# Performance work log

Hardware: AMD Instinct MI355X
Metric: run time of the kernel (lower is better)

Reference implementation:

```python
import jax, jax.numpy as jnp
import numpy as np

# LSNNParameters defaults (norse)
TAU_SYN_INV = 200.0     # 1/tau_syn
TAU_MEM_INV = 100.0     # 1/tau_mem
TAU_ADAPT_INV = 1.0 / 800.0  # 1/tau_adapt
V_LEAK = 0.0
V_TH = 1.0
V_RESET = 0.0
BETA = 1.8
DT = 0.001

B, IN_F, OUT_F = 8192, 512, 1024


def setup_inputs() -> dict:
    key = jax.random.key(0)
    k0, k1, k2, k3, k4, k5, k6 = jax.random.split(key, 7)
    input_spikes = (jax.random.uniform(k0, (B, IN_F)) < 0.2).astype(jnp.float32)
    z = (jax.random.uniform(k1, (B, OUT_F)) < 0.2).astype(jnp.float32)
    v = jax.random.normal(k2, (B, OUT_F)) * 0.5
    i = jax.random.normal(k3, (B, OUT_F)) * 0.5
    b = jax.random.uniform(k4, (B, OUT_F))
    input_weights = jax.random.normal(k5, (OUT_F, IN_F)) / np.sqrt(IN_F)
    recurrent_weights = jax.random.normal(k6, (OUT_F, OUT_F))
    return {
        "input_spikes": input_spikes,
        "z": z,
        "v": v,
        "i": i,
        "b": b,
        "input_weights": input_weights,
        "recurrent_weights": recurrent_weights,
    }


def reference(input_spikes, z, v, i, b, input_weights, recurrent_weights):
    # One euler step of the LSNN cell (norse lsnn_step).
    # voltage update: dv = dt * tau_mem_inv * ((v_leak - v) + i)
    v_decayed = v + DT * TAU_MEM_INV * ((V_LEAK - v) + i)
    # current decay: di = -dt * tau_syn_inv * i
    i_decayed = i + DT * (-TAU_SYN_INV) * i
    # adaptive threshold relaxes toward v_th
    b_decayed = b + DT * TAU_ADAPT_INV * (V_TH - b)
    # spike condition (heaviside jump)
    z_new = (v_decayed - b_decayed > 0).astype(v.dtype)
    # reset
    v_new = (1.0 - z_new) * v_decayed + z_new * V_RESET
    # current jumps from input + recurrent synapses (x @ W^T, torch linear)
    i_new = (
        i_decayed
        + jnp.einsum("bi,oi->bo", input_spikes, input_weights)
        + jnp.einsum("bo,no->bn", z, recurrent_weights)
    )
    # threshold adaptation
    b_new = b_decayed + z_new * TAU_ADAPT_INV * BETA
    # stack (z, v, i, b) new state -> [4, B, OUT_F]
    return jnp.stack([z_new, v_new, i_new, b_new])
```

## Files before the change

kernel.cpp:

```cpp
#include <hip/hip_runtime.h>

#define B_ROWS 8192
#define IN_F 512
#define OUT_F 1024
#define K_TOT 1536

#define BM 64
#define BN 64
#define BK 64
#define NITER (K_TOT / BK)

#define A4_COUNT (B_ROWS * (K_TOT / 4))
#define W4_COUNT (OUT_F  * (K_TOT / 4))

typedef short bfrag __attribute__((ext_vector_type(8)));
typedef float f4    __attribute__((ext_vector_type(4)));

__device__ __forceinline__ unsigned int pack2bf(float a, float b) {
    unsigned int ua = __float_as_uint(a);
    unsigned int ub = __float_as_uint(b);
    ua = (ua + 0x7fffu + ((ua >> 16) & 1u)) >> 16;
    ub = (ub + 0x7fffu + ((ub >> 16) & 1u)) & 0xffff0000u;
    return ua | ub;
}

__global__ __launch_bounds__(256) void precast(
    const float* __restrict__ spikes, const float* __restrict__ zin,
    const float* __restrict__ Wi,     const float* __restrict__ Wr,
    unsigned short* __restrict__ Abf, unsigned short* __restrict__ Wbf)
{
    const int idx = blockIdx.x * 256 + threadIdx.x;
    const float* src;
    unsigned short* dst;
    if (idx < A4_COUNT) {
        const int row = idx / 384, c4 = idx - row * 384;
        src = (c4 < 128) ? spikes + (size_t)row * IN_F + c4 * 4
                         : zin    + (size_t)row * OUT_F + (c4 - 128) * 4;
        dst = Abf + (size_t)idx * 4;
    } else {
        const int w = idx - A4_COUNT;
        const int row = w / 384, c4 = w - row * 384;
        src = (c4 < 128) ? Wi + (size_t)row * IN_F + c4 * 4
                         : Wr + (size_t)row * OUT_F + (c4 - 128) * 4;
        dst = Wbf + (size_t)w * 4;
    }
    const float4 v = *(const float4*)src;
    uint2 pk = { pack2bf(v.x, v.y), pack2bf(v.z, v.w) };
    *(uint2*)dst = pk;
}

__global__ __launch_bounds__(256, 8) void lsnn_gemm(
    const unsigned short* __restrict__ Abf,
    const unsigned short* __restrict__ Wbf,
    const float* __restrict__ vin,
    const float* __restrict__ iin,
    const float* __restrict__ bin,
    float* __restrict__ out)
{
    __shared__ unsigned short As[BM * BK];
    __shared__ unsigned short Ws[BN * BK];

    const int tid = threadIdx.x;
    const int bid = blockIdx.x;
    const int n0 = (bid & 15) * BN;
    const int m0 = (bid >> 4) * BM;

    const int lane = tid & 63;
    const int wave = tid >> 6;
    const int wm = (wave >> 1) * 32;
    const int wn = (wave & 1) * 32;
    const int lr = lane & 15;
    const int lq = lane >> 4;

    f4 acc[2][2];
    #pragma unroll
    for (int a = 0; a < 2; ++a)
        #pragma unroll
        for (int b = 0; b < 2; ++b)
            acc[a][b] = (f4)0.0f;

    const unsigned short* Ab = Abf + (size_t)m0 * K_TOT;
    const unsigned short* Wb = Wbf + (size_t)n0 * K_TOT;

    for (int it = 0; it < NITER; ++it) {
        const int kt = it * BK;
        __syncthreads();

        #pragma unroll
        for (int p = 0; p < 2; ++p) {
            const int j0 = p * 256 + wave * 64;
            const int q  = j0 + lane;
            const int r = q >> 3, s = q & 7, c = s ^ (r & 7);
            __builtin_amdgcn_global_load_lds(
                (const __attribute__((address_space(1))) void*)(Ab + (size_t)r * K_TOT + kt + c * 8),
                (__attribute__((address_space(3))) void*)(As + j0 * 8),
                16, 0, 0);
        }
        #pragma unroll
        for (int p = 0; p < 2; ++p) {
            const int j0 = p * 256 + wave * 64;
            const int q  = j0 + lane;
            const int r = q >> 3, s = q & 7, c = s ^ (r & 7);
            __builtin_amdgcn_global_load_lds(
                (const __attribute__((address_space(1))) void*)(Wb + (size_t)r * K_TOT + kt + c * 8),
                (__attribute__((address_space(3))) void*)(Ws + j0 * 8),
                16, 0, 0);
        }
        __syncthreads();

        #pragma unroll
        for (int ks = 0; ks < 2; ++ks) {
            const int cc = ks * 4 + lq;
            bfrag af[2], wf[2];
            #pragma unroll
            for (int t = 0; t < 2; ++t) {
                const int row = wm + t * 16 + lr;
                af[t] = *(const bfrag*)&As[row * BK + (cc ^ (row & 7)) * 8];
            }
            #pragma unroll
            for (int t = 0; t < 2; ++t) {
                const int row = wn + t * 16 + lr;
                wf[t] = *(const bfrag*)&Ws[row * BK + (cc ^ (row & 7)) * 8];
            }
            #pragma unroll
            for (int tm = 0; tm < 2; ++tm)
                #pragma unroll
                for (int tn = 0; tn < 2; ++tn)
                    acc[tm][tn] = __builtin_amdgcn_mfma_f32_16x16x32_bf16(
                        af[tm], wf[tn], acc[tm][tn], 0, 0, 0);
        }
    }

    const size_t PL = (size_t)B_ROWS * OUT_F;
    #pragma unroll
    for (int tm = 0; tm < 2; ++tm) {
        #pragma unroll
        for (int tn = 0; tn < 2; ++tn) {
            #pragma unroll
            for (int r = 0; r < 4; ++r) {
                const int gm = m0 + wm + tm * 16 + lq * 4 + r;
                const int gn = n0 + wn + tn * 16 + lr;
                const size_t idx = (size_t)gm * OUT_F + gn;
                const float v = vin[idx];
                const float i = iin[idx];
                const float b = bin[idx];
                const float v_dec = v + 0.1f * ((0.0f - v) + i);
                const float i_dec = i - 0.2f * i;
                const float b_dec = b + 1.25e-06f * (1.0f - b);
                const float zn = (v_dec - b_dec > 0.0f) ? 1.0f : 0.0f;
                const float vn = (1.0f - zn) * v_dec;
                const float inew = i_dec + acc[tm][tn][r];
                const float bnew = b_dec + zn * 0.00225f;
                out[idx]          = zn;
                out[PL + idx]     = vn;
                out[2 * PL + idx] = inew;
                out[3 * PL + idx] = bnew;
            }
        }
    }
}

extern "C" void kernel_launch(void* const* d_in, const int* in_sizes, int n_in,
                              void* d_out, int out_size, void* d_ws, size_t ws_size,
                              hipStream_t stream) {
    const float* spikes = (const float*)d_in[0];
    const float* z      = (const float*)d_in[1];
    const float* v      = (const float*)d_in[2];
    const float* i      = (const float*)d_in[3];
    const float* b      = (const float*)d_in[4];
    const float* Wi     = (const float*)d_in[5];
    const float* Wr     = (const float*)d_in[6];
    float* out = (float*)d_out;

    unsigned short* Abf = (unsigned short*)d_ws;
    unsigned short* Wbf = Abf + (size_t)B_ROWS * K_TOT;

    const int pc_grid = (A4_COUNT + W4_COUNT) / 256;
    precast<<<pc_grid, 256, 0, stream>>>(spikes, z, Wi, Wr, Abf, Wbf);

    const int grid = (B_ROWS / BM) * (OUT_F / BN);
    lsnn_gemm<<<grid, 256, 0, stream>>>(Abf, Wbf, v, i, b, out);
}
```

Measured before the change: 312.8 us.

## Fuse activation bf16 cast into GEMM with register-prefetched double-buffered LDS

```diff
diff --git a/kernel.cpp b/kernel.cpp
--- a/kernel.cpp
+++ b/kernel.cpp
@@ -10,13 +10,12 @@
 #define BK 64
 #define NITER (K_TOT / BK)
 
-#define A4_COUNT (B_ROWS * (K_TOT / 4))
-#define W4_COUNT (OUT_F  * (K_TOT / 4))
+#define W4_COUNT (OUT_F * (K_TOT / 4))
 
 typedef short bfrag __attribute__((ext_vector_type(8)));
 typedef float f4    __attribute__((ext_vector_type(4)));
 
-__device__ __forceinline__ unsigned int pack2bf(float a, float b) {
+__device__ __forceinline__ unsigned int pack2bf_rne(float a, float b) {
     unsigned int ua = __float_as_uint(a);
     unsigned int ub = __float_as_uint(b);
     ua = (ua + 0x7fffu + ((ua >> 16) & 1u)) >> 16;
@@ -24,41 +23,34 @@
     return ua | ub;
 }
 
-__global__ __launch_bounds__(256) void precast(
-    const float* __restrict__ spikes, const float* __restrict__ zin,
-    const float* __restrict__ Wi,     const float* __restrict__ Wr,
-    unsigned short* __restrict__ Abf, unsigned short* __restrict__ Wbf)
+__device__ __forceinline__ unsigned int pack2bf_trunc(float a, float b) {
+    return (__float_as_uint(a) >> 16) | (__float_as_uint(b) & 0xffff0000u);
+}
+
+__global__ __launch_bounds__(256) void precast_w(
+    const float* __restrict__ Wi, const float* __restrict__ Wr,
+    unsigned short* __restrict__ Wbf)
 {
     const int idx = blockIdx.x * 256 + threadIdx.x;
-    const float* src;
-    unsigned short* dst;
-    if (idx < A4_COUNT) {
-        const int row = idx / 384, c4 = idx - row * 384;
-        src = (c4 < 128) ? spikes + (size_t)row * IN_F + c4 * 4
-                         : zin    + (size_t)row * OUT_F + (c4 - 128) * 4;
-        dst = Abf + (size_t)idx * 4;
-    } else {
-        const int w = idx - A4_COUNT;
-        const int row = w / 384, c4 = w - row * 384;
-        src = (c4 < 128) ? Wi + (size_t)row * IN_F + c4 * 4
-                         : Wr + (size_t)row * OUT_F + (c4 - 128) * 4;
-        dst = Wbf + (size_t)w * 4;
-    }
+    const int row = idx / 384, c4 = idx - row * 384;
+    const float* src = (c4 < 128) ? Wi + (size_t)row * IN_F + c4 * 4
+                                  : Wr + (size_t)row * OUT_F + (c4 - 128) * 4;
     const float4 v = *(const float4*)src;
-    uint2 pk = { pack2bf(v.x, v.y), pack2bf(v.z, v.w) };
-    *(uint2*)dst = pk;
-}
-
-__global__ __launch_bounds__(256, 8) void lsnn_gemm(
-    const unsigned short* __restrict__ Abf,
+    uint2 pk = { pack2bf_rne(v.x, v.y), pack2bf_rne(v.z, v.w) };
+    *(uint2*)(Wbf + (size_t)idx * 4) = pk;
+}
+
+__global__ __launch_bounds__(256, 4) void lsnn_gemm(
+    const float* __restrict__ spikes,
+    const float* __restrict__ zin,
     const unsigned short* __restrict__ Wbf,
     const float* __restrict__ vin,
     const float* __restrict__ iin,
     const float* __restrict__ bin,
     float* __restrict__ out)
 {
-    __shared__ unsigned short As[BM * BK];
-    __shared__ unsigned short Ws[BN * BK];
+    __shared__ unsigned short As[2][BM * BK];
+    __shared__ unsigned short Ws[2][BN * BK];
 
     const int tid = threadIdx.x;
     const int bid = blockIdx.x;
@@ -79,34 +71,60 @@
         for (int b = 0; b < 2; ++b)
             acc[a][b] = (f4)0.0f;
 
-    const unsigned short* Ab = Abf + (size_t)m0 * K_TOT;
     const unsigned short* Wb = Wbf + (size_t)n0 * K_TOT;
-
+    int wr_[2], wc_[2], wj_[2];
+    #pragma unroll
+    for (int p = 0; p < 2; ++p) {
+        const int q = p * 256 + wave * 64 + lane;
+        wr_[p] = q >> 3;
+        wc_[p] = (q & 7) ^ (wr_[p] & 7);
+        wj_[p] = p * 256 + wave * 64;
+    }
+
+    const int ar = tid >> 2;
+    const int aq = tid & 3;
+    const float* aS = spikes + (size_t)(m0 + ar) * IN_F  + aq * 16;
+    const float* aZ = zin    + (size_t)(m0 + ar) * OUT_F + aq * 16;
+    const int s0 = (((aq * 2 + 0) ^ (ar & 7)) << 3);
+    const int s1 = (((aq * 2 + 1) ^ (ar & 7)) << 3);
+    const int arow = ar * BK;
+
+    {
+        const float4* ap = (const float4*)aS;
+    }
+    const float4* ap0 = (const float4*)aS;
+    float4 a0 = ap0[0], a1 = ap0[1], a2 = ap0[2], a3 = ap0[3];
+
+    int cur = 0;
     for (int it = 0; it < NITER; ++it) {
         const int kt = it * BK;
-        __syncthreads();
+        __builtin_amdgcn_sched_barrier(0);
+
+        uint4 pk0, pk1;
+        pk0.x = pack2bf_trunc(a0.x, a0.y); pk0.y = pack2bf_trunc(a0.z, a0.w);
+        pk0.z = pack2bf_trunc(a1.x, a1.y); pk0.w = pack2bf_trunc(a1.z, a1.w);
+        pk1.x = pack2bf_trunc(a2.x, a2.y); pk1.y = pack2bf_trunc(a2.z, a2.w);
+        pk1.z = pack2bf_trunc(a3.x, a3.y); pk1.w = pack2bf_trunc(a3.z, a3.w);
+        *(uint4*)&As[cur][arow + s0] = pk0;
+        *(uint4*)&As[cur][arow + s1] = pk1;
+        __builtin_amdgcn_sched_barrier(0);
 
         #pragma unroll
         for (int p = 0; p < 2; ++p) {
-            const int j0 = p * 256 + wave * 64;
-            const int q  = j0 + lane;
-            const int r = q >> 3, s = q & 7, c = s ^ (r & 7);
             __builtin_amdgcn_global_load_lds(
-                (const __attribute__((address_space(1))) void*)(Ab + (size_t)r * K_TOT + kt + c * 8),
-                (__attribute__((address_space(3))) void*)(As + j0 * 8),
+                (const __attribute__((address_space(1))) void*)(Wb + (size_t)wr_[p] * K_TOT + kt + wc_[p] * 8),
+                (__attribute__((address_space(3))) void*)(&Ws[cur][wj_[p] * 8]),
                 16, 0, 0);
         }
-        #pragma unroll
-        for (int p = 0; p < 2; ++p) {
-            const int j0 = p * 256 + wave * 64;
-            const int q  = j0 + lane;
-            const int r = q >> 3, s = q & 7, c = s ^ (r & 7);
-            __builtin_amdgcn_global_load_lds(
-                (const __attribute__((address_space(1))) void*)(Wb + (size_t)r * K_TOT + kt + c * 8),
-                (__attribute__((address_space(3))) void*)(Ws + j0 * 8),
-                16, 0, 0);
-        }
-        __syncthreads();
+        __builtin_amdgcn_sched_barrier(0);
+
+        const int kn = (it + 1 < NITER) ? kt + BK : 0;
+        const float4* an = (const float4*)((kn < IN_F) ? (aS + kn) : (aZ + (kn - IN_F)));
+        a0 = an[0]; a1 = an[1]; a2 = an[2]; a3 = an[3];
+        __builtin_amdgcn_sched_barrier(0);
+
+        asm volatile("s_waitcnt vmcnt(4) lgkmcnt(0)" ::: "memory");
+        __builtin_amdgcn_s_barrier();
 
         #pragma unroll
         for (int ks = 0; ks < 2; ++ks) {
@@ -115,12 +133,12 @@
             #pragma unroll
             for (int t = 0; t < 2; ++t) {
                 const int row = wm + t * 16 + lr;
-                af[t] = *(const bfrag*)&As[row * BK + (cc ^ (row & 7)) * 8];
+                af[t] = *(const bfrag*)&As[cur][row * BK + ((cc ^ (row & 7)) << 3)];
             }
             #pragma unroll
             for (int t = 0; t < 2; ++t) {
                 const int row = wn + t * 16 + lr;
-                wf[t] = *(const bfrag*)&Ws[row * BK + (cc ^ (row & 7)) * 8];
+                wf[t] = *(const bfrag*)&Ws[cur][row * BK + ((cc ^ (row & 7)) << 3)];
             }
             #pragma unroll
             for (int tm = 0; tm < 2; ++tm)
@@ -129,6 +147,7 @@
                     acc[tm][tn] = __builtin_amdgcn_mfma_f32_16x16x32_bf16(
                         af[tm], wf[tn], acc[tm][tn], 0, 0, 0);
         }
+        cur ^= 1;
     }
 
     const size_t PL = (size_t)B_ROWS * OUT_F;
@@ -172,12 +191,10 @@
     const float* Wr     = (const float*)d_in[6];
     float* out = (float*)d_out;
 
-    unsigned short* Abf = (unsigned short*)d_ws;
-    unsigned short* Wbf = Abf + (size_t)B_ROWS * K_TOT;
-
-    const int pc_grid = (A4_COUNT + W4_COUNT) / 256;
-    precast<<<pc_grid, 256, 0, stream>>>(spikes, z, Wi, Wr, Abf, Wbf);
+    unsigned short* Wbf = (unsigned short*)d_ws;
+
+    precast_w<<<W4_COUNT / 256, 256, 0, stream>>>(Wi, Wr, Wbf);
 
     const int grid = (B_ROWS / BM) * (OUT_F / BN);
-    lsnn_gemm<<<grid, 256, 0, stream>>>(Abf, Wbf, v, i, b, out);
-}
+    lsnn_gemm<<<grid, 256, 0, stream>>>(spikes, z, Wbf, v, i, b, out);
+}
```

After: 330.7 us. 5.7% more time.

## Double-buffer GEMM LDS tiles and move pointwise state updates into precast kernel

Applied to the files above, without the earlier changes.

```diff
diff --git a/kernel.cpp b/kernel.cpp
--- a/kernel.cpp
+++ b/kernel.cpp
@@ -12,6 +12,8 @@
 
 #define A4_COUNT (B_ROWS * (K_TOT / 4))
 #define W4_COUNT (OUT_F  * (K_TOT / 4))
+#define P4_COUNT (B_ROWS * OUT_F / 4)
+#define PRE_TASKS (A4_COUNT + W4_COUNT + P4_COUNT)
 
 typedef short bfrag __attribute__((ext_vector_type(8)));
 typedef float f4    __attribute__((ext_vector_type(4)));
@@ -24,41 +26,82 @@
     return ua | ub;
 }
 
-__global__ __launch_bounds__(256) void precast(
+__global__ __launch_bounds__(256) void precast_pointwise(
     const float* __restrict__ spikes, const float* __restrict__ zin,
     const float* __restrict__ Wi,     const float* __restrict__ Wr,
-    unsigned short* __restrict__ Abf, unsigned short* __restrict__ Wbf)
+    const float* __restrict__ vin,    const float* __restrict__ iin,
+    const float* __restrict__ bin,
+    unsigned short* __restrict__ Abf, unsigned short* __restrict__ Wbf,
+    float* __restrict__ out)
 {
     const int idx = blockIdx.x * 256 + threadIdx.x;
-    const float* src;
-    unsigned short* dst;
-    if (idx < A4_COUNT) {
-        const int row = idx / 384, c4 = idx - row * 384;
-        src = (c4 < 128) ? spikes + (size_t)row * IN_F + c4 * 4
-                         : zin    + (size_t)row * OUT_F + (c4 - 128) * 4;
-        dst = Abf + (size_t)idx * 4;
+    if (idx < A4_COUNT + W4_COUNT) {
+        const float* src;
+        unsigned short* dst;
+        if (idx < A4_COUNT) {
+            const int row = idx / 384, c4 = idx - row * 384;
+            src = (c4 < 128) ? spikes + (size_t)row * IN_F + c4 * 4
+                             : zin    + (size_t)row * OUT_F + (c4 - 128) * 4;
+            dst = Abf + (size_t)idx * 4;
+        } else {
+            const int w = idx - A4_COUNT;
+            const int row = w / 384, c4 = w - row * 384;
+            src = (c4 < 128) ? Wi + (size_t)row * IN_F + c4 * 4
+                             : Wr + (size_t)row * OUT_F + (c4 - 128) * 4;
+            dst = Wbf + (size_t)w * 4;
+        }
+        const float4 v = *(const float4*)src;
+        uint2 pk = { pack2bf(v.x, v.y), pack2bf(v.z, v.w) };
+        *(uint2*)dst = pk;
     } else {
-        const int w = idx - A4_COUNT;
-        const int row = w / 384, c4 = w - row * 384;
-        src = (c4 < 128) ? Wi + (size_t)row * IN_F + c4 * 4
-                         : Wr + (size_t)row * OUT_F + (c4 - 128) * 4;
-        dst = Wbf + (size_t)w * 4;
-    }
-    const float4 v = *(const float4*)src;
-    uint2 pk = { pack2bf(v.x, v.y), pack2bf(v.z, v.w) };
-    *(uint2*)dst = pk;
-}
-
-__global__ __launch_bounds__(256, 8) void lsnn_gemm(
+        const int j = idx - (A4_COUNT + W4_COUNT);
+        const size_t PL = (size_t)B_ROWS * OUT_F;
+        const float4 v = ((const float4*)vin)[j];
+        const float4 i = ((const float4*)iin)[j];
+        const float4 b = ((const float4*)bin)[j];
+        float4 z, vn, bn;
+        {
+            const float v_dec = v.x + 0.1f * ((0.0f - v.x) + i.x);
+            const float b_dec = b.x + 1.25e-06f * (1.0f - b.x);
+            z.x = (v_dec - b_dec > 0.0f) ? 1.0f : 0.0f;
+            vn.x = (1.0f - z.x) * v_dec;
+            bn.x = b_dec + z.x * 0.00225f;
+        }
+        {
+            const float v_dec = v.y + 0.1f * ((0.0f - v.y) + i.y);
+            const float b_dec = b.y + 1.25e-06f * (1.0f - b.y);
+            z.y = (v_dec - b_dec > 0.0f) ? 1.0f : 0.0f;
+            vn.y = (1.0f - z.y) * v_dec;
+            bn.y = b_dec + z.y * 0.00225f;
+        }
+        {
+            const float v_dec = v.z + 0.1f * ((0.0f - v.z) + i.z);
+            const float b_dec = b.z + 1.25e-06f * (1.0f - b.z);
+            z.z = (v_dec - b_dec > 0.0f) ? 1.0f : 0.0f;
+            vn.z = (1.0f - z.z) * v_dec;
+            bn.z = b_dec + z.z * 0.00225f;
+        }
+        {
+            const float v_dec = v.w + 0.1f * ((0.0f - v.w) + i.w);
+            const float b_dec = b.w + 1.25e-06f * (1.0f - b.w);
+            z.w = (v_dec - b_dec > 0.0f) ? 1.0f : 0.0f;
+            vn.w = (1.0f - z.w) * v_dec;
+            bn.w = b_dec + z.w * 0.00225f;
+        }
+        ((float4*)out)[j]            = z;
+        ((float4*)(out + PL))[j]     = vn;
+        ((float4*)(out + 3 * PL))[j] = bn;
+    }
+}
+
+__global__ __launch_bounds__(256, 4) void lsnn_gemm(
     const unsigned short* __restrict__ Abf,
     const unsigned short* __restrict__ Wbf,
-    const float* __restrict__ vin,
     const float* __restrict__ iin,
-    const float* __restrict__ bin,
     float* __restrict__ out)
 {
-    __shared__ unsigned short As[BM * BK];
-    __shared__ unsigned short Ws[BN * BK];
+    __shared__ unsigned short As[2][BM * BK];
+    __shared__ unsigned short Ws[2][BN * BK];
 
     const int tid = threadIdx.x;
     const int bid = blockIdx.x;
@@ -82,31 +125,36 @@
     const unsigned short* Ab = Abf + (size_t)m0 * K_TOT;
     const unsigned short* Wb = Wbf + (size_t)n0 * K_TOT;
 
+    int rr[2], cc_[2], jj[2];
+    #pragma unroll
+    for (int p = 0; p < 2; ++p) {
+        const int q = p * 256 + wave * 64 + lane;
+        rr[p] = q >> 3;
+        cc_[p] = (q & 7) ^ (rr[p] & 7);
+        jj[p] = p * 256 + wave * 64;
+    }
+
+    auto stage = [&](int buf, int kt) {
+        #pragma unroll
+        for (int p = 0; p < 2; ++p)
+            __builtin_amdgcn_global_load_lds(
+                (const __attribute__((address_space(1))) void*)(Ab + (size_t)rr[p] * K_TOT + kt + cc_[p] * 8),
+                (__attribute__((address_space(3))) void*)(&As[buf][jj[p] * 8]),
+                16, 0, 0);
+        #pragma unroll
+        for (int p = 0; p < 2; ++p)
+            __builtin_amdgcn_global_load_lds(
+                (const __attribute__((address_space(1))) void*)(Wb + (size_t)rr[p] * K_TOT + kt + cc_[p] * 8),
+                (__attribute__((address_space(3))) void*)(&Ws[buf][jj[p] * 8]),
+                16, 0, 0);
+    };
+
+    stage(0, 0);
+    __syncthreads();
+
+    int cur = 0;
     for (int it = 0; it < NITER; ++it) {
-        const int kt = it * BK;
-        __syncthreads();
-
-        #pragma unroll
-        for (int p = 0; p < 2; ++p) {
-            const int j0 = p * 256 + wave * 64;
-            const int q  = j0 + lane;
-            const int r = q >> 3, s = q & 7, c = s ^ (r & 7);
-            __builtin_amdgcn_global_load_lds(
-                (const __attribute__((address_space(1))) void*)(Ab + (size_t)r * K_TOT + kt + c * 8),
-                (__attribute__((address_space(3))) void*)(As + j0 * 8),
-                16, 0, 0);
-        }
-        #pragma unroll
-        for (int p = 0; p < 2; ++p) {
-            const int j0 = p * 256 + wave * 64;
-            const int q  = j0 + lane;
-            const int r = q >> 3, s = q & 7, c = s ^ (r & 7);
-            __builtin_amdgcn_global_load_lds(
-                (const __attribute__((address_space(1))) void*)(Wb + (size_t)r * K_TOT + kt + c * 8),
-                (__attribute__((address_space(3))) void*)(Ws + j0 * 8),
-                16, 0, 0);
-        }
-        __syncthreads();
+        if (it + 1 < NITER) stage(cur ^ 1, (it + 1) * BK);
 
         #pragma unroll
         for (int ks = 0; ks < 2; ++ks) {
@@ -115,12 +163,12 @@
             #pragma unroll
             for (int t = 0; t < 2; ++t) {
                 const int row = wm + t * 16 + lr;
-                af[t] = *(const bfrag*)&As[row * BK + (cc ^ (row & 7)) * 8];
+                af[t] = *(const bfrag*)&As[cur][row * BK + ((cc ^ (row & 7)) << 3)];
             }
             #pragma unroll
             for (int t = 0; t < 2; ++t) {
                 const int row = wn + t * 16 + lr;
-                wf[t] = *(const bfrag*)&Ws[row * BK + (cc ^ (row & 7)) * 8];
+                wf[t] = *(const bfrag*)&Ws[cur][row * BK + ((cc ^ (row & 7)) << 3)];
             }
             #pragma unroll
             for (int tm = 0; tm < 2; ++tm)
@@ -129,9 +177,12 @@
                     acc[tm][tn] = __builtin_amdgcn_mfma_f32_16x16x32_bf16(
                         af[tm], wf[tn], acc[tm][tn], 0, 0, 0);
         }
-    }
-
-    const size_t PL = (size_t)B_ROWS * OUT_F;
+
+        __syncthreads();
+        cur ^= 1;
+    }
+
+    const size_t PL2 = 2 * (size_t)B_ROWS * OUT_F;
     #pragma unroll
     for (int tm = 0; tm < 2; ++tm) {
         #pragma unroll
@@ -141,20 +192,8 @@
                 const int gm = m0 + wm + tm * 16 + lq * 4 + r;
                 const int gn = n0 + wn + tn * 16 + lr;
                 const size_t idx = (size_t)gm * OUT_F + gn;
-                const float v = vin[idx];
                 const float i = iin[idx];
-                const float b = bin[idx];
-                const float v_dec = v + 0.1f * ((0.0f - v) + i);
-                const float i_dec = i - 0.2f * i;
-                const float b_dec = b + 1.25e-06f * (1.0f - b);
-                const float zn = (v_dec - b_dec > 0.0f) ? 1.0f : 0.0f;
-                const float vn = (1.0f - zn) * v_dec;
-                const float inew = i_dec + acc[tm][tn][r];
-                const float bnew = b_dec + zn * 0.00225f;
-                out[idx]          = zn;
-                out[PL + idx]     = vn;
-                out[2 * PL + idx] = inew;
-                out[3 * PL + idx] = bnew;
+                out[PL2 + idx] = (i - 0.2f * i) + acc[tm][tn][r];
             }
         }
     }
@@ -175,9 +214,9 @@
     unsigned short* Abf = (unsigned short*)d_ws;
     unsigned short* Wbf = Abf + (size_t)B_ROWS * K_TOT;
 
-    const int pc_grid = (A4_COUNT + W4_COUNT) / 256;
-    precast<<<pc_grid, 256, 0, stream>>>(spikes, z, Wi, Wr, Abf, Wbf);
+    precast_pointwise<<<PRE_TASKS / 256, 256, 0, stream>>>(
+        spikes, z, Wi, Wr, v, i, b, Abf, Wbf, out);
 
     const int grid = (B_ROWS / BM) * (OUT_F / BN);
-    lsnn_gemm<<<grid, 256, 0, stream>>>(Abf, Wbf, v, i, b, out);
-}
+    lsnn_gemm<<<grid, 256, 0, stream>>>(Abf, Wbf, i, out);
+}
```

Result: no change. 308.5 us (-1.4%).
